# Performance work log

Measured on AMD Instinct MI355X. Metric: run time of the kernel, lower is better.

The kernel has to match this reference:

```python
import jax, jax.numpy as jnp
import numpy as np

H = 12  # num_heads (init_kwargs)


def setup_inputs() -> dict:
    key = jax.random.key(0)
    ks = jax.random.split(key, 8)
    B, N, W = 32, 576, 16      # batch, num patches, local window
    d, P = 768, 4              # d_model, num_prompts
    s = lambda k, shape: jax.random.normal(k, shape, jnp.float32) * 0.02
    return dict(
        x=jax.random.normal(ks[0], (B, N, 1536), jnp.float32),
        y=jax.random.normal(ks[1], (B, N * W, 1024), jnp.float32),
        Wx=s(ks[2], (d, 1536)), bx=jnp.zeros((d,), jnp.float32),
        Wy=s(ks[3], (d, 1024)), by=jnp.zeros((d,), jnp.float32),
        prompt=jax.random.normal(ks[4], (1, P, d), jnp.float32),
        in_proj_w=s(ks[5], (3 * d, d)), in_proj_b=jnp.zeros((3 * d,), jnp.float32),
        out_w=s(ks[6], (d, d)), out_b=jnp.zeros((d,), jnp.float32),
    )


def reference(x, y, Wx, bx, Wy, by, prompt, in_proj_w, in_proj_b, out_w, out_b):
    B, N, _ = x.shape
    d = Wx.shape[0]
    W = y.shape[1] // N          # local kv window = 16
    P = prompt.shape[1]          # num prompts
    Dh = d // H
    scale = 1.0 / float(np.sqrt(Dh))

    x_proj = x @ Wx.T + bx                      # [B,N,d]
    y_proj = (y @ Wy.T + by).reshape(B, N, W, d)  # [B,N,W,d] local kv windows

    # queries per patch i: [x_proj[:, i], prompts] -> [B,N,1+P,d]
    pr = jnp.broadcast_to(prompt[:, None], (B, N, P, d))
    q_in = jnp.concatenate([x_proj[:, :, None, :], pr], axis=2)

    Wq, Wk, Wv = jnp.split(in_proj_w, 3, axis=0)
    bq, bk, bv = jnp.split(in_proj_b, 3)
    q = (q_in @ Wq.T + bq).reshape(B, N, 1 + P, H, Dh)
    k = (y_proj @ Wk.T + bk).reshape(B, N, W, H, Dh)
    v = (y_proj @ Wv.T + bv).reshape(B, N, W, H, Dh)

    scores = jnp.einsum('bnqhd,bnkhd->bnhqk', q, k) * scale  # [B,N,H,1+P,W]
    attn = jax.nn.softmax(scores, axis=-1)
    o = jnp.einsum('bnhqk,bnkhd->bnqhd', attn, v).reshape(B, N, 1 + P, d)
    out = o @ out_w.T + out_b                   # [B,N,1+P,d]
    return out.reshape(B, N * (1 + P), d)
```

## Files before the change

### kernel.cpp

```cpp
#include <hip/hip_runtime.h>
#include <hip/hip_bf16.h>


typedef __attribute__((ext_vector_type(8))) short bf16x8;
typedef __attribute__((ext_vector_type(4))) float f32x4;
typedef __attribute__((ext_vector_type(2))) float f32x2;
typedef __attribute__((ext_vector_type(8))) unsigned short u16x8;

__device__ __forceinline__ float bf2f(unsigned short u) {
  union { unsigned int i; float f; } x; x.i = ((unsigned int)u) << 16; return x.f;
}
__device__ __forceinline__ unsigned short f2b(float f) {
  union { float f; unsigned int i; } x; x.f = f;
  unsigned int u = x.i;
  return (unsigned short)((u + 0x7fffu + ((u >> 16) & 1u)) >> 16);
}
__device__ __forceinline__ unsigned int cvtpk(float lo, float hi) {
  unsigned int r;
  asm("v_cvt_pk_bf16_f32 %0, %1, %2" : "=v"(r) : "v"(lo), "v"(hi));
  return r;
}
__device__ __forceinline__ f32x2 bf2x(unsigned int u) {
  union { unsigned int i; float f; } lo, hi;
  lo.i = u << 16; hi.i = u & 0xFFFF0000u;
  f32x2 r; r[0] = lo.f; r[1] = hi.f; return r;
}
__device__ __forceinline__ void pkfma(f32x2& acc, f32x2 a, f32x2 b) {
  asm("v_pk_fma_f32 %0, %1, %2, %0" : "+v"(acc) : "v"(a), "v"(b));
}

#define GLDS(gaddr, laddr) \
  __builtin_amdgcn_global_load_lds( \
      (const __attribute__((address_space(1))) unsigned int*)(gaddr), \
      (__attribute__((address_space(3))) unsigned int*)(laddr), 16, 0, 0)

__global__ void k_cvt(const float* __restrict__ src, unsigned short* __restrict__ dst, long n8) {
  long stride = (long)gridDim.x * blockDim.x;
  for (long i = (long)blockIdx.x * blockDim.x + threadIdx.x; i < n8; i += stride) {
    float4 a = ((const float4*)src)[2 * i];
    float4 b = ((const float4*)src)[2 * i + 1];
    u16x8 t = { f2b(a.x), f2b(a.y), f2b(a.z), f2b(a.w),
                f2b(b.x), f2b(b.y), f2b(b.z), f2b(b.w) };
    ((u16x8*)dst)[i] = t;
  }
}

__global__ __launch_bounds__(256) void k_tr(const float* __restrict__ src,
                                            unsigned short* __restrict__ dst,
                                            int R, int C) {
  __shared__ float t[32][33];
  int bx = blockIdx.x * 32, by = blockIdx.y * 32;
  int lx = threadIdx.x & 31, ly = threadIdx.x >> 5;
#pragma unroll
  for (int s = 0; s < 32; s += 8)
    t[ly + s][lx] = src[(long)(by + ly + s) * C + bx + lx];
  __syncthreads();
#pragma unroll
  for (int s = 0; s < 32; s += 8)
    dst[(long)(bx + ly + s) * R + by + lx] = f2b(t[lx][ly + s]);
}

__global__ void k_zf(float* __restrict__ p, int n) {
  int i = blockIdx.x * 256 + threadIdx.x;
  if (i < n) p[i] = 0.f;
}

__global__ void k_bfuse(const float* __restrict__ ipw, const float* __restrict__ ipb,
                        const float* __restrict__ bx, const float* __restrict__ by,
                        float* __restrict__ bqx, float* __restrict__ bkv) {
  int o    = blockIdx.x * 4 + (threadIdx.x >> 6);
  int lane = threadIdx.x & 63;
  int sec  = o / 768, jj = o - sec * 768;
  const float* Arow = ipw + (long)o * 768;
  const float* vb   = (sec == 0) ? bx : by;
  float s = 0.f;
  for (int k = lane; k < 768; k += 64) s += Arow[k] * vb[k];
#pragma unroll
  for (int d = 32; d > 0; d >>= 1) s += __shfl_down(s, d);
  if (lane == 0) {
    s += ipb[o];
    if (sec == 0) bqx[jj] = s;
    else if (sec == 1) bkv[jj] = s;
    else bkv[768 + jj] = s;
  }
}

__global__ void k_qprompt(const float* __restrict__ ipw, const float* __restrict__ ipb,
                          const float* __restrict__ prompt, unsigned short* __restrict__ qpf) {
  int o    = blockIdx.x * 4 + (threadIdx.x >> 6);
  int lane = threadIdx.x & 63;
  int p = o / 768, j = o - p * 768;
  const float* Wqr = ipw + (long)j * 768;
  const float* pr  = prompt + (long)p * 768;
  float s = 0.f;
  for (int k = lane; k < 768; k += 64) s += Wqr[k] * pr[k];
#pragma unroll
  for (int d = 32; d > 0; d >>= 1) s += __shfl_down(s, d);
  if (lane == 0) qpf[o] = f2b(s + ipb[j]);
}

template <typename OutT>
__global__ __launch_bounds__(256) void k_gemm(const unsigned short* __restrict__ A,
                                              const unsigned short* __restrict__ Bw,
                                              const float* __restrict__ bias,
                                              OutT* __restrict__ C,
                                              int M, int Nn, int K, int nbx) {
  const int tid  = threadIdx.x;
  const int lane = tid & 63, wid = tid >> 6;
  const int wm = wid >> 1, wn = wid & 1;
  const int lr = lane & 15, lk = lane >> 4;

  const int nwg = gridDim.x, orig = blockIdx.x;
  const int q8 = nwg >> 3, r8 = nwg & 7, xc = orig & 7;
  const int wg = (xc < r8 ? xc * (q8 + 1) : r8 * (q8 + 1) + (xc - r8) * q8) + (orig >> 3);
  const int bn = wg % nbx, bm = wg / nbx;
  const int m0 = bm * 128, n0 = bn * 128;

  __shared__ __attribute__((aligned(16))) unsigned short As[2][128 * 32];
  __shared__ __attribute__((aligned(16))) unsigned short Bs[2][128 * 32];

  f32x4 acc[4][4];
#pragma unroll
  for (int nt = 0; nt < 4; ++nt) {
    float bv = bias[n0 + wn * 64 + nt * 16 + lr];
    f32x4 bvv = {bv, bv, bv, bv};
#pragma unroll
    for (int mt = 0; mt < 4; ++mt) acc[mt][nt] = bvv;
  }

  const int NS = K >> 5;
  const int crow = lane >> 2, ck8 = (lane & 3) * 8;

  auto stage = [&](int buf, int ks) {
#pragma unroll
    for (int i = 0; i < 2; ++i) {
      int c = wid * 2 + i;
      int row = c * 16 + crow;
      GLDS(&A[(long)(m0 + row) * K + ks * 32 + ck8], &As[buf][c * 512]);
      GLDS(&Bw[(long)(n0 + row) * K + ks * 32 + ck8], &Bs[buf][c * 512]);
    }
  };

  stage(0, 0);
  __syncthreads();

  for (int t = 0; t < NS; ++t) {
    const int cur = t & 1, nb = cur ^ 1;
    if (t + 1 < NS) stage(nb, t + 1);
    bf16x8 af[4], bfr[4];
#pragma unroll
    for (int mt = 0; mt < 4; ++mt)
      af[mt] = *(const bf16x8*)&As[cur][(wm * 64 + mt * 16 + lr) * 32 + lk * 8];
#pragma unroll
    for (int nt = 0; nt < 4; ++nt)
      bfr[nt] = *(const bf16x8*)&Bs[cur][(wn * 64 + nt * 16 + lr) * 32 + lk * 8];
#pragma unroll
    for (int mt = 0; mt < 4; ++mt)
#pragma unroll
      for (int nt = 0; nt < 4; ++nt)
        acc[mt][nt] = __builtin_amdgcn_mfma_f32_16x16x32_bf16(af[mt], bfr[nt], acc[mt][nt], 0, 0, 0);
    __syncthreads();
  }

#pragma unroll
  for (int mt = 0; mt < 4; ++mt)
#pragma unroll
    for (int nt = 0; nt < 4; ++nt) {
      int col = n0 + wn * 64 + nt * 16 + lr;
#pragma unroll
      for (int r = 0; r < 4; ++r) {
        int row = m0 + wm * 64 + mt * 16 + lk * 4 + r;
        float v = acc[mt][nt][r];
        if constexpr (sizeof(OutT) == 4) C[(long)row * Nn + col] = v;
        else                             C[(long)row * Nn + col] = f2b(v);
      }
    }
}

template <bool KVL, typename OutT>
__global__ __launch_bounds__(512, 2) void k_gemm8(const unsigned short* __restrict__ A,
                                                  const unsigned short* __restrict__ Bw,
                                                  const float* __restrict__ bias,
                                                  OutT* __restrict__ C,
                                                  int M, int Nn, int K, int nbx) {
  const int tid  = threadIdx.x;
  const int lane = tid & 63, wid = tid >> 6;
  const int wm = wid >> 2, wn = wid & 3;
  const int lr = lane & 15, lk = lane >> 4;

  const int nwg = gridDim.x, orig = blockIdx.x;
  const int q8 = nwg >> 3, r8 = nwg & 7, xc = orig & 7;
  const int wg = (xc < r8 ? xc * (q8 + 1) : r8 * (q8 + 1) + (xc - r8) * q8) + (orig >> 3);
  const int bn = wg % nbx, bm = wg / nbx;
  const long m0 = (long)bm * 256, n0 = (long)bn * 256;

  __shared__ __attribute__((aligned(16))) unsigned short As[2][2][8192];
  __shared__ __attribute__((aligned(16))) unsigned short Bs[2][2][8192];

  f32x4 acc[8][4];
#pragma unroll
  for (int nt = 0; nt < 4; ++nt) {
    float bv = bias[n0 + wn * 64 + nt * 16 + lr];
    f32x4 bvv = {bv, bv, bv, bv};
#pragma unroll
    for (int mt = 0; mt < 8; ++mt) acc[mt][nt] = bvv;
  }

  const int NT = K >> 6;

  auto stage = [&](int buf, int kt, int isB, int h) {
#pragma unroll
    for (int j = 0; j < 2; ++j) {
      int c   = j * 8 + wid;
      int row = c * 8 + (lane >> 3);
      int col = ((lane & 7) * 8) ^ ((row & 7) << 3);
      const unsigned short* g = isB
          ? &Bw[(n0 + h * 128 + row) * (long)K + kt * 64 + col]
          : &A [(m0 + h * 128 + row) * (long)K + kt * 64 + col];
      unsigned short* l = isB ? &Bs[buf][h][c * 512] : &As[buf][h][c * 512];
      GLDS(g, l);
    }
  };
  auto ldsA = [&](int buf, int mt, int kk) -> bf16x8 {
    int r = mt * 16 + lr;
    int off = r * 128 + ((kk * 64 + lk * 16) ^ ((lr & 7) << 4));
    return *(const bf16x8*)((const char*)&As[buf][wm][0] + off);
  };
  auto ldsB = [&](int buf, int nt, int kk) -> bf16x8 {
    int r = (wn & 1) * 64 + nt * 16 + lr;
    int off = r * 128 + ((kk * 64 + lk * 16) ^ ((lr & 7) << 4));
    return *(const bf16x8*)((const char*)&Bs[buf][wn >> 1][0] + off);
  };

  stage(0, 0, 0, 0); stage(0, 0, 0, 1); stage(0, 0, 1, 0); stage(0, 0, 1, 1);
  if (NT > 1) {
    stage(1, 1, 0, 0);
    asm volatile("s_waitcnt vmcnt(2)" ::: "memory");
  } else {
    asm volatile("s_waitcnt vmcnt(0)" ::: "memory");
  }
  __builtin_amdgcn_s_barrier();

  for (int u = 0; u < NT; ++u) {
    const int cb = u & 1;
    bf16x8 a[4][2], b0[2][2], b1[2][2];

#pragma unroll
    for (int mt = 0; mt < 4; ++mt) { a[mt][0] = ldsA(cb, mt, 0); a[mt][1] = ldsA(cb, mt, 1); }
#pragma unroll
    for (int nt = 0; nt < 2; ++nt) { b0[nt][0] = ldsB(cb, nt, 0); b0[nt][1] = ldsB(cb, nt, 1); }
    if (u + 1 < NT) stage(cb ^ 1, u + 1, 0, 1);
    __builtin_amdgcn_s_barrier();
    asm volatile("s_waitcnt lgkmcnt(0)" ::: "memory");
    __builtin_amdgcn_s_setprio(1);
#pragma unroll
    for (int mt = 0; mt < 4; ++mt)
#pragma unroll
      for (int nt = 0; nt < 2; ++nt)
#pragma unroll
        for (int kk = 0; kk < 2; ++kk)
          acc[mt][nt] = __builtin_amdgcn_mfma_f32_16x16x32_bf16(a[mt][kk], b0[nt][kk], acc[mt][nt], 0, 0, 0);
    __builtin_amdgcn_s_setprio(0);
    __builtin_amdgcn_s_barrier();

#pragma unroll
    for (int nt = 0; nt < 2; ++nt) { b1[nt][0] = ldsB(cb, 2 + nt, 0); b1[nt][1] = ldsB(cb, 2 + nt, 1); }
    if (u + 1 < NT) stage(cb ^ 1, u + 1, 1, 0);
    __builtin_amdgcn_s_barrier();
    asm volatile("s_waitcnt lgkmcnt(0)" ::: "memory");
    __builtin_amdgcn_s_setprio(1);
#pragma unroll
    for (int mt = 0; mt < 4; ++mt)
#pragma unroll
      for (int nt = 0; nt < 2; ++nt)
#pragma unroll
        for (int kk = 0; kk < 2; ++kk)
          acc[mt][2 + nt] = __builtin_amdgcn_mfma_f32_16x16x32_bf16(a[mt][kk], b1[nt][kk], acc[mt][2 + nt], 0, 0, 0);
    __builtin_amdgcn_s_setprio(0);
    __builtin_amdgcn_s_barrier();

#pragma unroll
    for (int mt = 0; mt < 4; ++mt) { a[mt][0] = ldsA(cb, 4 + mt, 0); a[mt][1] = ldsA(cb, 4 + mt, 1); }
    if (u + 1 < NT) stage(cb ^ 1, u + 1, 1, 1);
    __builtin_amdgcn_s_barrier();
    asm volatile("s_waitcnt lgkmcnt(0)" ::: "memory");
    __builtin_amdgcn_s_setprio(1);
#pragma unroll
    for (int mt = 0; mt < 4; ++mt)
#pragma unroll
      for (int nt = 0; nt < 2; ++nt)
#pragma unroll
        for (int kk = 0; kk < 2; ++kk)
          acc[4 + mt][2 + nt] = __builtin_amdgcn_mfma_f32_16x16x32_bf16(a[mt][kk], b1[nt][kk], acc[4 + mt][2 + nt], 0, 0, 0);
    __builtin_amdgcn_s_setprio(0);
    __builtin_amdgcn_s_barrier();

    if (u + 2 < NT) stage(cb, u + 2, 0, 0);
    __builtin_amdgcn_s_barrier();
    __builtin_amdgcn_s_setprio(1);
#pragma unroll
    for (int mt = 0; mt < 4; ++mt)
#pragma unroll
      for (int nt = 0; nt < 2; ++nt)
#pragma unroll
        for (int kk = 0; kk < 2; ++kk)
          acc[4 + mt][nt] = __builtin_amdgcn_mfma_f32_16x16x32_bf16(a[mt][kk], b0[nt][kk], acc[4 + mt][nt], 0, 0, 0);
    __builtin_amdgcn_s_setprio(0);
    if (u + 2 < NT)       asm volatile("s_waitcnt vmcnt(2)" ::: "memory");
    else if (u + 1 < NT)  asm volatile("s_waitcnt vmcnt(0)" ::: "memory");
    __builtin_amdgcn_s_barrier();
  }

#pragma unroll
  for (int mt = 0; mt < 8; ++mt)
#pragma unroll
    for (int nt = 0; nt < 4; ++nt) {
      long col = n0 + wn * 64 + nt * 16 + lr;
#pragma unroll
      for (int r = 0; r < 4; ++r) {
        long row = m0 + wm * 128 + mt * 16 + lk * 4 + r;
        float v = acc[mt][nt][r];
        if constexpr (KVL) {
          long pp = row >> 4; int w = (int)(row & 15);
          long addr;
          if (col < 768) addr = pp * 24576 + (col >> 6) * 1024 + w * 64 + (col & 63);
          else           addr = pp * 24576 + 12288 + (long)w * 768 + (col - 768);
          C[addr] = f2b(v);
        } else if constexpr (sizeof(OutT) == 4) {
          C[row * Nn + col] = v;
        } else {
          C[row * Nn + col] = f2b(v);
        }
      }
    }
}

__global__ __launch_bounds__(256, 6) void k_attn(const unsigned short* __restrict__ kv,
                                                 const unsigned short* __restrict__ qx,
                                                 const unsigned short* __restrict__ qp,
                                                 unsigned short* __restrict__ o) {
  __shared__ __attribute__((aligned(16))) unsigned short Qs[5 * 768];
  __shared__ float Ss[60 * 16];
  const int tid = threadIdx.x;
  const long pp = (long)blockIdx.x;

  for (int i = tid; i < 5 * 96; i += 256) {
    int r = i / 96, c8 = i - r * 96;
    const unsigned short* src = (r == 0) ? &qx[pp * 768 + c8 * 8]
                                         : &qp[(long)(r - 1) * 768 + c8 * 8];
    *(u16x8*)&Qs[r * 768 + c8 * 8] = *(const u16x8*)src;
  }
  __syncthreads();

  if (tid < 192) {
    const int h = tid >> 4, w = tid & 15;
    const uint4* kr = (const uint4*)&kv[pp * 24576 + h * 1024 + w * 64];
    f32x2 s2[5];
#pragma unroll
    for (int q5 = 0; q5 < 5; ++q5) { s2[q5][0] = 0.f; s2[q5][1] = 0.f; }
#pragma unroll
    for (int half = 0; half < 2; ++half) {
      uint4 kk0 = kr[half * 4 + 0], kk1 = kr[half * 4 + 1],
            kk2 = kr[half * 4 + 2], kk3 = kr[half * 4 + 3];
#pragma unroll
      for (int q5 = 0; q5 < 5; ++q5) {
        const uint4* qr = (const uint4*)&Qs[q5 * 768 + h * 64 + half * 32];
#pragma unroll
        for (int j = 0; j < 4; ++j) {
          uint4 kkj = (j == 0) ? kk0 : (j == 1) ? kk1 : (j == 2) ? kk2 : kk3;
          uint4 qw = qr[j];
          pkfma(s2[q5], bf2x(kkj.x), bf2x(qw.x));
          pkfma(s2[q5], bf2x(kkj.y), bf2x(qw.y));
          pkfma(s2[q5], bf2x(kkj.z), bf2x(qw.z));
          pkfma(s2[q5], bf2x(kkj.w), bf2x(qw.w));
        }
      }
    }
#pragma unroll
    for (int q5 = 0; q5 < 5; ++q5) {
      float s = (s2[q5][0] + s2[q5][1]) * 0.125f;
      float m = s;
#pragma unroll
      for (int d = 1; d < 16; d <<= 1) m = fmaxf(m, __shfl_xor(m, d));
      float e = __expf(s - m);
      float sum = e;
#pragma unroll
      for (int d = 1; d < 16; d <<= 1) sum += __shfl_xor(sum, d);
      Ss[(q5 * 12 + h) * 16 + w] = e / sum;
    }
  }
  __syncthreads();

  for (int idx = tid; idx < 480; idx += 256) {
    int d8 = idx % 96, q5 = idx / 96;
    int h = d8 >> 3;
    const float* arow = &Ss[(q5 * 12 + h) * 16];
    const unsigned short* vbase = &kv[pp * 24576 + 12288 + d8 * 8];
    f32x2 a0 = {0.f, 0.f}, a1 = {0.f, 0.f}, a2v = {0.f, 0.f}, a3 = {0.f, 0.f};
#pragma unroll
    for (int w = 0; w < 16; ++w) {
      uint4 vv = *(const uint4*)&vbase[(long)w * 768];
      float aw = arow[w];
      f32x2 aw2 = {aw, aw};
      pkfma(a0,  bf2x(vv.x), aw2);
      pkfma(a1,  bf2x(vv.y), aw2);
      pkfma(a2v, bf2x(vv.z), aw2);
      pkfma(a3,  bf2x(vv.w), aw2);
    }
    uint4 pk;
    pk.x = cvtpk(a0[0],  a0[1]);
    pk.y = cvtpk(a1[0],  a1[1]);
    pk.z = cvtpk(a2v[0], a2v[1]);
    pk.w = cvtpk(a3[0],  a3[1]);
    *(uint4*)&o[(pp * 5 + q5) * 768 + d8 * 8] = pk;
  }
}

extern "C" void kernel_launch(void* const* d_in, const int* in_sizes, int n_in,
                              void* d_out, int out_size, void* d_ws, size_t ws_size,
                              hipStream_t stream) {
  const float* x      = (const float*)d_in[0];
  const float* y      = (const float*)d_in[1];
  const float* Wx     = (const float*)d_in[2];
  const float* bx     = (const float*)d_in[3];
  const float* Wy     = (const float*)d_in[4];
  const float* by     = (const float*)d_in[5];
  const float* prompt = (const float*)d_in[6];
  const float* ipw    = (const float*)d_in[7];
  const float* ipb    = (const float*)d_in[8];
  const float* outw   = (const float*)d_in[9];
  const float* outb   = (const float*)d_in[10];
  float* out = (float*)d_out;

  char* ws = (char*)d_ws;
  size_t off = 0;
  auto alloc = [&](size_t bytes) -> void* {
    void* p = ws + off; off += (bytes + 255) & ~(size_t)255; return p;
  };
  unsigned short* kvb  = (unsigned short*)alloc(294912UL * 1536 * 2);
  unsigned short* qxb  = (unsigned short*)alloc(18432UL * 768 * 2);
  unsigned short* ob   = (unsigned short*)alloc(92160UL * 768 * 2);
  unsigned short* Wqx  = (unsigned short*)alloc(768UL * 1536 * 2);
  unsigned short* Wkv  = (unsigned short*)alloc(1536UL * 1024 * 2);
  unsigned short* oww  = (unsigned short*)alloc(768UL * 768 * 2);
  unsigned short* qpf  = (unsigned short*)alloc(4UL * 768 * 2);
  float*          bqx  = (float*)alloc(768 * 4);
  float*          bkv  = (float*)alloc(1536 * 4);
  unsigned short* ipwb = (unsigned short*)alloc(2304UL * 768 * 2);
  unsigned short* WxT  = (unsigned short*)alloc(1536UL * 768 * 2);
  unsigned short* WyT  = (unsigned short*)alloc(1024UL * 768 * 2);
  float*          zb   = (float*)alloc(1536 * 4);
  unsigned short* xb   = ob;
  unsigned short* ybc  = (unsigned short*)(ws + off);
  long rpc = (long)((ws_size - off) / (1024 * 2)) & ~255L;
  if (rpc > 294912) rpc = 294912;
  if (rpc < 256) rpc = 256;

  k_cvt<<<dim3(288), dim3(256), 0, stream>>>(outw, oww, 768L * 768 / 8);
  k_cvt<<<dim3(864), dim3(256), 0, stream>>>(ipw, ipwb, 2304L * 768 / 8);
  k_tr<<<dim3(48, 24), dim3(256), 0, stream>>>(Wx, WxT, 768, 1536);
  k_tr<<<dim3(32, 24), dim3(256), 0, stream>>>(Wy, WyT, 768, 1024);
  k_zf<<<dim3(6), dim3(256), 0, stream>>>(zb, 1536);
  k_gemm<unsigned short><<<dim3(6 * 12), dim3(256), 0, stream>>>(
      ipwb, WxT, zb, Wqx, 768, 1536, 768, 12);
  k_gemm<unsigned short><<<dim3(6 * 8), dim3(256), 0, stream>>>(
      ipwb + 768 * 768, WyT, zb, Wkv, 768, 1024, 768, 8);
  k_gemm<unsigned short><<<dim3(6 * 8), dim3(256), 0, stream>>>(
      ipwb + 1536 * 768, WyT, zb, Wkv + 768 * 1024, 768, 1024, 768, 8);
  k_bfuse<<<dim3(576), dim3(256), 0, stream>>>(ipw, ipb, bx, by, bqx, bkv);
  k_qprompt<<<dim3(768), dim3(256), 0, stream>>>(ipw, ipb, prompt, qpf);

  k_cvt<<<dim3(2048), dim3(256), 0, stream>>>(x, xb, 18432L * 1536 / 8);
  k_gemm<unsigned short><<<dim3(144 * 6), dim3(256), 0, stream>>>(
      xb, Wqx, bqx, qxb, 18432, 768, 1536, 6);

  long row0 = 0;
  while (row0 < 294912) {
    long mc = 294912 - row0 < rpc ? 294912 - row0 : rpc;
    k_cvt<<<dim3(2048), dim3(256), 0, stream>>>(y + row0 * 1024, ybc, mc * 128);
    k_gemm8<true, unsigned short><<<dim3((int)(mc / 256) * 6), dim3(512), 0, stream>>>(
        ybc, Wkv, bkv, kvb + row0 * 1536, (int)mc, 1536, 1024, 6);
    row0 += mc;
  }

  k_attn<<<dim3(18432), dim3(256), 0, stream>>>(kvb, qxb, qpf, ob);

  k_gemm8<false, float><<<dim3(360 * 3), dim3(512), 0, stream>>>(
      ob, oww, outb, out, 92160, 768, 768, 3);
}
```

Measured before the change: 2.101 ms.

## Overlap y bf16 conversion with KV GEMM via fused double-buffered kernel

The per-chunk y fp32→bf16 conversion is folded into the KV GEMM launch: extra workgroups convert the next chunk into a second buffer while the GEMM processes the current one, and chunks are capped at 73728 rows. The KV GEMM epilogue now writes plain row-major output instead of the scattered head-major layout, and the attention kernel's K/V addressing is changed to match. Softmax is split into a separate shared-memory pass after the scores are written. This aims to hide conversion time and coalesce GEMM stores. In exchange it adds more launches, contends with the GEMM for bandwidth, and gives attention K loads a strided access pattern.

```diff
diff --git a/kernel.cpp b/kernel.cpp
--- a/kernel.cpp
+++ b/kernel.cpp
@@ -34,15 +34,21 @@
       (const __attribute__((address_space(1))) unsigned int*)(gaddr), \
       (__attribute__((address_space(3))) unsigned int*)(laddr), 16, 0, 0)
 
-__global__ void k_cvt(const float* __restrict__ src, unsigned short* __restrict__ dst, long n8) {
-  long stride = (long)gridDim.x * blockDim.x;
-  for (long i = (long)blockIdx.x * blockDim.x + threadIdx.x; i < n8; i += stride) {
+__device__ __forceinline__ void cvt_body(const float* __restrict__ src,
+                                         unsigned short* __restrict__ dst,
+                                         long n8, long start, long stride) {
+  for (long i = start; i < n8; i += stride) {
     float4 a = ((const float4*)src)[2 * i];
     float4 b = ((const float4*)src)[2 * i + 1];
     u16x8 t = { f2b(a.x), f2b(a.y), f2b(a.z), f2b(a.w),
                 f2b(b.x), f2b(b.y), f2b(b.z), f2b(b.w) };
     ((u16x8*)dst)[i] = t;
   }
+}
+
+__global__ void k_cvt(const float* __restrict__ src, unsigned short* __restrict__ dst, long n8) {
+  cvt_body(src, dst, n8, (long)blockIdx.x * blockDim.x + threadIdx.x,
+           (long)gridDim.x * blockDim.x);
 }
 
 __global__ __launch_bounds__(256) void k_tr(const float* __restrict__ src,
@@ -177,18 +183,18 @@
     }
 }
 
-template <bool KVL, typename OutT>
-__global__ __launch_bounds__(512, 2) void k_gemm8(const unsigned short* __restrict__ A,
-                                                  const unsigned short* __restrict__ Bw,
-                                                  const float* __restrict__ bias,
-                                                  OutT* __restrict__ C,
-                                                  int M, int Nn, int K, int nbx) {
+template <typename OutT>
+__device__ __forceinline__ void gemm8_body(const unsigned short* __restrict__ A,
+                                           const unsigned short* __restrict__ Bw,
+                                           const float* __restrict__ bias,
+                                           OutT* __restrict__ C,
+                                           int M, int Nn, int K, int nbx,
+                                           int orig, int nwg) {
   const int tid  = threadIdx.x;
   const int lane = tid & 63, wid = tid >> 6;
   const int wm = wid >> 2, wn = wid & 3;
   const int lr = lane & 15, lk = lane >> 4;
 
-  const int nwg = gridDim.x, orig = blockIdx.x;
   const int q8 = nwg >> 3, r8 = nwg & 7, xc = orig & 7;
   const int wg = (xc < r8 ? xc * (q8 + 1) : r8 * (q8 + 1) + (xc - r8) * q8) + (orig >> 3);
   const int bn = wg % nbx, bm = wg / nbx;
@@ -320,19 +326,35 @@
       for (int r = 0; r < 4; ++r) {
         long row = m0 + wm * 128 + mt * 16 + lk * 4 + r;
         float v = acc[mt][nt][r];
-        if constexpr (KVL) {
-          long pp = row >> 4; int w = (int)(row & 15);
-          long addr;
-          if (col < 768) addr = pp * 24576 + (col >> 6) * 1024 + w * 64 + (col & 63);
-          else           addr = pp * 24576 + 12288 + (long)w * 768 + (col - 768);
-          C[addr] = f2b(v);
-        } else if constexpr (sizeof(OutT) == 4) {
-          C[row * Nn + col] = v;
-        } else {
-          C[row * Nn + col] = f2b(v);
-        }
+        if constexpr (sizeof(OutT) == 4) C[row * Nn + col] = v;
+        else                             C[row * Nn + col] = f2b(v);
       }
     }
+}
+
+template <typename OutT>
+__global__ __launch_bounds__(512, 2) void k_gemm8(const unsigned short* __restrict__ A,
+                                                  const unsigned short* __restrict__ Bw,
+                                                  const float* __restrict__ bias,
+                                                  OutT* __restrict__ C,
+                                                  int M, int Nn, int K, int nbx) {
+  gemm8_body<OutT>(A, Bw, bias, C, M, Nn, K, nbx, blockIdx.x, gridDim.x);
+}
+
+__global__ __launch_bounds__(512, 2) void k_kvfat(const unsigned short* __restrict__ A,
+                                                  const unsigned short* __restrict__ Bw,
+                                                  const float* __restrict__ bias,
+                                                  unsigned short* __restrict__ C,
+                                                  int M, int Nn, int K, int nbx,
+                                                  const float* __restrict__ ysrc,
+                                                  unsigned short* __restrict__ ydst,
+                                                  long n8, int ncvt) {
+  if ((int)blockIdx.x < ncvt) {
+    cvt_body(ysrc, ydst, n8, (long)blockIdx.x * 512 + threadIdx.x, (long)ncvt * 512);
+    return;
+  }
+  gemm8_body<unsigned short>(A, Bw, bias, C, M, Nn, K, nbx,
+                             (int)blockIdx.x - ncvt, (int)gridDim.x - ncvt);
 }
 
 __global__ __launch_bounds__(256, 6) void k_attn(const unsigned short* __restrict__ kv,
@@ -353,8 +375,8 @@
   __syncthreads();
 
   if (tid < 192) {
-    const int h = tid >> 4, w = tid & 15;
-    const uint4* kr = (const uint4*)&kv[pp * 24576 + h * 1024 + w * 64];
+    const int w = tid / 12, h = tid - (tid / 12) * 12;
+    const uint4* kr = (const uint4*)&kv[(pp * 16 + w) * 1536 + h * 64];
     f32x2 s2[5];
 #pragma unroll
     for (int q5 = 0; q5 < 5; ++q5) { s2[q5][0] = 0.f; s2[q5][1] = 0.f; }
@@ -377,17 +399,22 @@
       }
     }
 #pragma unroll
-    for (int q5 = 0; q5 < 5; ++q5) {
-      float s = (s2[q5][0] + s2[q5][1]) * 0.125f;
-      float m = s;
-#pragma unroll
-      for (int d = 1; d < 16; d <<= 1) m = fmaxf(m, __shfl_xor(m, d));
-      float e = __expf(s - m);
-      float sum = e;
-#pragma unroll
-      for (int d = 1; d < 16; d <<= 1) sum += __shfl_xor(sum, d);
-      Ss[(q5 * 12 + h) * 16 + w] = e / sum;
-    }
+    for (int q5 = 0; q5 < 5; ++q5)
+      Ss[(q5 * 12 + h) * 16 + w] = (s2[q5][0] + s2[q5][1]) * 0.125f;
+  }
+  __syncthreads();
+
+  for (int idx = tid; idx < 960; idx += 256) {
+    int w = idx & 15, rest = idx >> 4;
+    float s = Ss[rest * 16 + w];
+    float m = s;
+#pragma unroll
+    for (int d = 1; d < 16; d <<= 1) m = fmaxf(m, __shfl_xor(m, d));
+    float e = __expf(s - m);
+    float sum = e;
+#pragma unroll
+    for (int d = 1; d < 16; d <<= 1) sum += __shfl_xor(sum, d);
+    Ss[rest * 16 + w] = e / sum;
   }
   __syncthreads();
 
@@ -395,11 +422,11 @@
     int d8 = idx % 96, q5 = idx / 96;
     int h = d8 >> 3;
     const float* arow = &Ss[(q5 * 12 + h) * 16];
-    const unsigned short* vbase = &kv[pp * 24576 + 12288 + d8 * 8];
+    const unsigned short* vbase = &kv[pp * 24576 + 768 + d8 * 8];
     f32x2 a0 = {0.f, 0.f}, a1 = {0.f, 0.f}, a2v = {0.f, 0.f}, a3 = {0.f, 0.f};
 #pragma unroll
     for (int w = 0; w < 16; ++w) {
-      uint4 vv = *(const uint4*)&vbase[(long)w * 768];
+      uint4 vv = *(const uint4*)&vbase[(long)w * 1536];
       float aw = arow[w];
       f32x2 aw2 = {aw, aw};
       pkfma(a0,  bf2x(vv.x), aw2);
@@ -451,10 +478,12 @@
   unsigned short* WyT  = (unsigned short*)alloc(1024UL * 768 * 2);
   float*          zb   = (float*)alloc(1536 * 4);
   unsigned short* xb   = ob;
-  unsigned short* ybc  = (unsigned short*)(ws + off);
-  long rpc = (long)((ws_size - off) / (1024 * 2)) & ~255L;
-  if (rpc > 294912) rpc = 294912;
+
+  long rpc = (long)((ws_size - off) / (1024 * 2 * 2)) & ~255L;
+  if (rpc > 73728) rpc = 73728;
   if (rpc < 256) rpc = 256;
+  unsigned short* ybc0 = (unsigned short*)(ws + off);
+  unsigned short* ybc1 = ybc0 + rpc * 1024;
 
   k_cvt<<<dim3(288), dim3(256), 0, stream>>>(outw, oww, 768L * 768 / 8);
   k_cvt<<<dim3(864), dim3(256), 0, stream>>>(ipw, ipwb, 2304L * 768 / 8);
@@ -474,17 +503,27 @@
   k_gemm<unsigned short><<<dim3(144 * 6), dim3(256), 0, stream>>>(
       xb, Wqx, bqx, qxb, 18432, 768, 1536, 6);
 
-  long row0 = 0;
-  while (row0 < 294912) {
-    long mc = 294912 - row0 < rpc ? 294912 - row0 : rpc;
-    k_cvt<<<dim3(2048), dim3(256), 0, stream>>>(y + row0 * 1024, ybc, mc * 128);
-    k_gemm8<true, unsigned short><<<dim3((int)(mc / 256) * 6), dim3(512), 0, stream>>>(
-        ybc, Wkv, bkv, kvb + row0 * 1536, (int)mc, 1536, 1024, 6);
-    row0 += mc;
+  {
+    long mc0 = 294912 < rpc ? 294912 : rpc;
+    k_cvt<<<dim3(2048), dim3(256), 0, stream>>>(y, ybc0, mc0 * 128);
+    long row0 = 0; int pi = 0;
+    while (row0 < 294912) {
+      long mc = 294912 - row0 < rpc ? 294912 - row0 : rpc;
+      long next0 = row0 + mc;
+      long mcn = (next0 < 294912) ? ((294912 - next0 < rpc) ? 294912 - next0 : rpc) : 0;
+      int ngemm = (int)(mc / 256) * 6;
+      int ncvt  = mcn ? 128 : 0;
+      unsigned short* cur = (pi & 1) ? ybc1 : ybc0;
+      unsigned short* nxt = (pi & 1) ? ybc0 : ybc1;
+      k_kvfat<<<dim3(ngemm + ncvt), dim3(512), 0, stream>>>(
+          cur, Wkv, bkv, kvb + row0 * 1536, (int)mc, 1536, 1024, 6,
+          y + next0 * 1024, nxt, mcn * 128, ncvt);
+      row0 = next0; ++pi;
+    }
   }
 
   k_attn<<<dim3(18432), dim3(256), 0, stream>>>(kvb, qxb, qpf, ob);
 
-  k_gemm8<false, float><<<dim3(360 * 3), dim3(512), 0, stream>>>(
+  k_gemm8<float><<<dim3(360 * 3), dim3(512), 0, stream>>>(
       ob, oww, outb, out, 92160, 768, 768, 3);
 }
```

New measurement: 1.958 ms. 1.07x faster.
